# Kernel optimization log

Measured on AMD Instinct MI355X. Metric: run time of the kernel, lower is better.

Reference implementation:

```python
import jax, jax.numpy as jnp
import numpy as np

D = 128  # d_pair
N = 512  # n_res
B = 1
EPS = 1e-5


def setup_inputs() -> dict:
    key = jax.random.key(0)
    ks = jax.random.split(key, 16)
    s = 0.02
    inp = {
        "pair": jax.random.normal(ks[0], (B, N, N, D), dtype=jnp.float32),
        "pair_mask": jnp.ones((B, N, N), dtype=jnp.float32),
        "ln_g": jnp.ones((D,), dtype=jnp.float32),
        "ln_b": jnp.zeros((D,), dtype=jnp.float32),
        "w_lp": jax.random.normal(ks[1], (D, D), dtype=jnp.float32) * s,
        "b_lp": jnp.zeros((D,), dtype=jnp.float32),
        "w_lg": jax.random.normal(ks[2], (D, D), dtype=jnp.float32) * s,
        "b_lg": jnp.zeros((D,), dtype=jnp.float32),
        "w_rp": jax.random.normal(ks[3], (D, D), dtype=jnp.float32) * s,
        "b_rp": jnp.zeros((D,), dtype=jnp.float32),
        "w_rg": jax.random.normal(ks[4], (D, D), dtype=jnp.float32) * s,
        "b_rg": jnp.zeros((D,), dtype=jnp.float32),
        "w_g": jax.random.normal(ks[5], (D, D), dtype=jnp.float32) * s,
        "b_g": jnp.zeros((D,), dtype=jnp.float32),
        "w_o": jax.random.normal(ks[6], (D, D), dtype=jnp.float32) * s,
        "b_o": jnp.zeros((D,), dtype=jnp.float32),
    }
    return inp


def _layer_norm(x, g, b):
    mu = jnp.mean(x, axis=-1, keepdims=True)
    var = jnp.mean(jnp.square(x - mu), axis=-1, keepdims=True)
    return (x - mu) * jax.lax.rsqrt(var + EPS) * g + b


def reference(pair, pair_mask, ln_g, ln_b, w_lp, b_lp, w_lg, b_lg,
              w_rp, b_rp, w_rg, b_rg, w_g, b_g, w_o, b_o):
    # [B,N,N,D] pair representation; outgoing triangle multiplication
    x = _layer_norm(pair, ln_g, ln_b)
    mask = pair_mask[..., None]  # [B,N,N,1]
    left = (x @ w_lp + b_lp) * jax.nn.sigmoid(x @ w_lg + b_lg) * mask
    right = (x @ w_rp + b_rp) * jax.nn.sigmoid(x @ w_rg + b_rg) * mask
    # outgoing: contract over j -> per-channel NxN matmul
    out = jnp.einsum('bijd,bjkd->bikd', left, right)
    out = out * jax.nn.sigmoid(x @ w_g + b_g)
    out = out @ w_o + b_o
    return out
```

## Files before the change

### kernel.cpp

```cpp
#include <hip/hip_runtime.h>

#define NN 512
#define DD 128
#define PP (NN*NN)

typedef __attribute__((ext_vector_type(8))) short short8;
typedef __attribute__((ext_vector_type(4))) short shortx4;
typedef __attribute__((ext_vector_type(4))) float floatx4;
typedef __attribute__((ext_vector_type(4))) unsigned int uintx4;

__device__ __forceinline__ unsigned short f2bf(float f) {
  unsigned int u = __float_as_uint(f);
  u += 0x7fffu + ((u >> 16) & 1u);
  return (unsigned short)(u >> 16);
}
__device__ __forceinline__ float bf2f(unsigned short h) {
  return __uint_as_float(((unsigned int)h) << 16);
}
__device__ __forceinline__ unsigned int pkbf2(float lo, float hi) {
  unsigned int r;
  asm("v_cvt_pk_bf16_f32 %0, %1, %2" : "=v"(r) : "v"(lo), "v"(hi));
  return r;
}
__device__ __forceinline__ float sigm(float x) {
  return 1.f / (1.f + __expf(-x));
}

__device__ __forceinline__ void gload_lds16(const unsigned short* g, unsigned short* l) {
  __builtin_amdgcn_global_load_lds(
      (const __attribute__((address_space(1))) unsigned int*)g,
      (__attribute__((address_space(3))) unsigned int*)l, 16, 0, 0);
}

__global__ void k0_prep(const float* __restrict__ wlp, const float* __restrict__ wlg,
                        const float* __restrict__ wrp, const float* __restrict__ wrg,
                        const float* __restrict__ wg,  const float* __restrict__ wo,
                        unsigned short* __restrict__ wt) {
  const float* src[6] = {wlp, wlg, wrp, wrg, wg, wo};
  int m = blockIdx.y;
  int idx = blockIdx.x * 256 + threadIdx.x;
  int d = idx >> 7, e = idx & 127;
  wt[m * 16384 + e * 128 + d] = f2bf(src[m][d * 128 + e]);
}

__launch_bounds__(256, 4)
__global__ void k1a_ln(const float* __restrict__ pair,
                       const float* __restrict__ lng, const float* __restrict__ lnb,
                       unsigned short* __restrict__ xln) {
  const int t = threadIdx.x;
  const long p0 = (long)blockIdx.x << 7;
  const int r = t >> 1, h = t & 1;
  const float* row = pair + (p0 + r) * DD + h * 64;
  floatx4 v[16];
  float s = 0.f, s2 = 0.f;
  #pragma unroll
  for (int c = 0; c < 16; ++c) {
    v[c] = *(const floatx4*)(row + c * 4);
    s  += v[c].x + v[c].y + v[c].z + v[c].w;
    s2 += v[c].x * v[c].x + v[c].y * v[c].y + v[c].z * v[c].z + v[c].w * v[c].w;
  }
  s  += __shfl_xor(s, 1);
  s2 += __shfl_xor(s2, 1);
  float mu = s * (1.f / 128.f);
  float var = s2 * (1.f / 128.f) - mu * mu;
  float rs = rsqrtf(var + 1e-5f);
  unsigned short* orow = xln + (p0 + r) * DD + h * 64;
  #pragma unroll
  for (int c2 = 0; c2 < 8; ++c2) {
    floatx4 g0 = *(const floatx4*)(lng + h * 64 + c2 * 8);
    floatx4 g1 = *(const floatx4*)(lng + h * 64 + c2 * 8 + 4);
    floatx4 b0 = *(const floatx4*)(lnb + h * 64 + c2 * 8);
    floatx4 b1 = *(const floatx4*)(lnb + h * 64 + c2 * 8 + 4);
    floatx4 a = v[2 * c2], b = v[2 * c2 + 1];
    uintx4 u;
    u[0] = pkbf2((a.x - mu) * rs * g0.x + b0.x, (a.y - mu) * rs * g0.y + b0.y);
    u[1] = pkbf2((a.z - mu) * rs * g0.z + b0.z, (a.w - mu) * rs * g0.w + b0.w);
    u[2] = pkbf2((b.x - mu) * rs * g1.x + b1.x, (b.y - mu) * rs * g1.y + b1.y);
    u[3] = pkbf2((b.z - mu) * rs * g1.z + b1.z, (b.w - mu) * rs * g1.w + b1.w);
    *(uintx4*)(orow + c2 * 8) = u;
  }
}

__launch_bounds__(256, 2)
__global__ void k1b_proj(const unsigned short* __restrict__ xln,
                         const float* __restrict__ pmask,
                         const unsigned short* __restrict__ wt,
                         const float* __restrict__ b_lp, const float* __restrict__ b_lg,
                         const float* __restrict__ b_rp, const float* __restrict__ b_rg,
                         const float* __restrict__ b_g,
                         unsigned short* __restrict__ left_t,
                         unsigned short* __restrict__ right_bt,
                         unsigned short* __restrict__ gate_t) {
  __shared__ __align__(16) unsigned short Sm[17408];
  __shared__ float Mlds[128];
  unsigned short* Al = Sm;
  unsigned short* Bp = Sm + 4096;
  unsigned short* Bg = Sm + 8192;

  const int t = threadIdx.x;
  const int unit = blockIdx.y;
  const int q = blockIdx.x;

  int j0 = 0, kk = 0;
  long p0 = 0, soff;
  if (unit == 1) {
    j0 = (q >> 9) << 7; kk = q & 511;
    soff = (long)kk * NN + j0;
  } else {
    p0 = (long)q << 7;
    soff = p0;
  }
  auto arow = [&](int r) -> long {
    return (unit == 1) ? ((long)(j0 + r) * NN + kk) : (p0 + r);
  };

  if (unit < 2 && t < 128) Mlds[t] = pmask[arow(t)];

  const unsigned short* wA = wt + (unit == 0 ? 0 : unit == 1 ? 2 : 4) * 16384;
  const unsigned short* wB = wt + (unit == 0 ? 1 : 3) * 16384;

  const int lane = t & 63, w = t >> 6;
  const int ln = lane & 15, q8 = lane >> 4;
  const int wm = (w >> 1) << 6, we = (w & 1) << 6;
  const int sr = t >> 2, sc = t & 3;

  floatx4 aP[4][4] = {}, aG[4][4] = {};
  for (int kc = 0; kc < 4; ++kc) {
    gload_lds16(xln + arow(sr) * DD + kc * 32 + sc * 8,      &Al[t * 8]);
    gload_lds16(xln + arow(sr + 64) * DD + kc * 32 + sc * 8, &Al[(256 + t) * 8]);
    gload_lds16(wA + sr * 128 + kc * 32 + sc * 8,            &Bp[t * 8]);
    gload_lds16(wA + (sr + 64) * 128 + kc * 32 + sc * 8,     &Bp[(256 + t) * 8]);
    if (unit < 2) {
      gload_lds16(wB + sr * 128 + kc * 32 + sc * 8,          &Bg[t * 8]);
      gload_lds16(wB + (sr + 64) * 128 + kc * 32 + sc * 8,   &Bg[(256 + t) * 8]);
    }
    __syncthreads();
    short8 a[4];
    #pragma unroll
    for (int i = 0; i < 4; ++i)
      a[i] = *(const short8*)&Al[(wm + i * 16 + ln) * 32 + q8 * 8];
    #pragma unroll
    for (int j = 0; j < 4; ++j) {
      short8 bpv = *(const short8*)&Bp[(we + j * 16 + ln) * 32 + q8 * 8];
      #pragma unroll
      for (int i = 0; i < 4; ++i)
        aP[i][j] = __builtin_amdgcn_mfma_f32_16x16x32_bf16(a[i], bpv, aP[i][j], 0, 0, 0);
    }
    if (unit < 2) {
      #pragma unroll
      for (int j = 0; j < 4; ++j) {
        short8 bgv = *(const short8*)&Bg[(we + j * 16 + ln) * 32 + q8 * 8];
        #pragma unroll
        for (int i = 0; i < 4; ++i)
          aG[i][j] = __builtin_amdgcn_mfma_f32_16x16x32_bf16(a[i], bgv, aG[i][j], 0, 0, 0);
      }
    }
    __syncthreads();
  }

  unsigned short* mystg = Sm + w * 4352;
  if (unit < 2) {
    const float* bpp = (unit == 0) ? b_lp : b_rp;
    const float* bgg = (unit == 0) ? b_lg : b_rg;
    #pragma unroll
    for (int j = 0; j < 4; ++j) {
      int eg = we + j * 16 + ln;
      float bp = bpp[eg], bg = bgg[eg];
      #pragma unroll
      for (int i = 0; i < 4; ++i) {
        float vv[4];
        #pragma unroll
        for (int r = 0; r < 4; ++r) {
          int m = wm + i * 16 + q8 * 4 + r;
          vv[r] = (aP[i][j][r] + bp) * sigm(aG[i][j][r] + bg) * Mlds[m];
        }
        unsigned int* du = (unsigned int*)&mystg[(j * 16 + ln) * 68 + i * 16 + q8 * 4];
        du[0] = pkbf2(vv[0], vv[1]);
        du[1] = pkbf2(vv[2], vv[3]);
      }
    }
  } else {
    #pragma unroll
    for (int j = 0; j < 4; ++j) {
      int eg = we + j * 16 + ln;
      float bg = b_g[eg];
      #pragma unroll
      for (int i = 0; i < 4; ++i) {
        float vv[4];
        #pragma unroll
        for (int r = 0; r < 4; ++r)
          vv[r] = sigm(aP[i][j][r] + bg);
        unsigned int* du = (unsigned int*)&mystg[(j * 16 + ln) * 68 + i * 16 + q8 * 4];
        du[0] = pkbf2(vv[0], vv[1]);
        du[1] = pkbf2(vv[2], vv[3]);
      }
    }
  }

  unsigned short* dstbase = (unit == 0) ? left_t : (unit == 1 ? right_bt : gate_t);
  #pragma unroll
  for (int itr = 0; itr < 8; ++itr) {
    int row = itr * 8 + (lane >> 3);
    int c = lane & 7;
    short8 vv = *(const short8*)&mystg[row * 68 + c * 8];
    long eg = we + row;
    *(short8*)(dstbase + eg * PP + soff + wm + c * 8) = vv;
  }
}

__launch_bounds__(256, 3)
__global__ void k2_einsum(const unsigned short* __restrict__ left_t,
                          const unsigned short* __restrict__ right_bt,
                          unsigned short* __restrict__ tmpg) {
  __shared__ __align__(16) unsigned short Sm[128 * 132];
  unsigned short* Al = Sm;
  unsigned short* Bl = Sm + 128 * 32;
  unsigned short* Cl = Sm;
  const int t = threadIdx.x;
  const int d = blockIdx.y;
  const int i0 = (blockIdx.x >> 2) << 7;
  const int k0 = (blockIdx.x & 3) << 7;
  const unsigned short* Ag = left_t   + (long)d * PP;
  const unsigned short* Bg = right_bt + (long)d * PP;
  const int lane = t & 63, w = t >> 6;
  const int ln = lane & 15, q8 = lane >> 4;
  const int wm = (w >> 1) << 6, wn = (w & 1) << 6;

  floatx4 acc[4][4] = {};
  for (int j0 = 0; j0 < NN; j0 += 32) {
    #pragma unroll
    for (int it = 0; it < 2; ++it) {
      int flat = it * 256 + t;
      int r = flat >> 2, c = flat & 3;
      gload_lds16(Ag + (long)(i0 + r) * NN + j0 + c * 8, &Al[flat * 8]);
    }
    #pragma unroll
    for (int it = 0; it < 2; ++it) {
      int flat = it * 256 + t;
      int r = flat >> 2, c = flat & 3;
      gload_lds16(Bg + (long)(k0 + r) * NN + j0 + c * 8, &Bl[flat * 8]);
    }
    __syncthreads();
    short8 a[4], b[4];
    #pragma unroll
    for (int i = 0; i < 4; ++i)
      a[i] = *(const short8*)&Al[(wm + i * 16 + ln) * 32 + q8 * 8];
    #pragma unroll
    for (int i = 0; i < 4; ++i)
      b[i] = *(const short8*)&Bl[(wn + i * 16 + ln) * 32 + q8 * 8];
    #pragma unroll
    for (int i = 0; i < 4; ++i)
      #pragma unroll
      for (int j = 0; j < 4; ++j)
        acc[i][j] = __builtin_amdgcn_mfma_f32_16x16x32_bf16(a[i], b[j], acc[i][j], 0, 0, 0);
    __syncthreads();
  }
  #pragma unroll
  for (int i = 0; i < 4; ++i)
    #pragma unroll
    for (int j = 0; j < 4; ++j) {
      int n = wn + j * 16 + ln;
      #pragma unroll
      for (int r = 0; r < 4; ++r)
        Cl[(wm + i * 16 + q8 * 4 + r) * 132 + n] = f2bf(acc[i][j][r]);
    }
  __syncthreads();
  unsigned short* Og = tmpg + (long)d * PP;
  #pragma unroll
  for (int it = 0; it < 8; ++it) {
    int flat = it * 256 + t;
    int m = flat >> 4, c = flat & 15;
    *(short8*)(Og + (long)(i0 + m) * NN + k0 + c * 8) = *(const short8*)&Cl[m * 132 + c * 8];
  }
}

__launch_bounds__(256, 3)
__global__ void k3_out(const unsigned short* __restrict__ tmpg,
                       const unsigned short* __restrict__ gate_t,
                       const unsigned short* __restrict__ wt,
                       const float* __restrict__ b_o,
                       float* __restrict__ out) {
  __shared__ __align__(16) unsigned short Tl[128 * 144];
  unsigned int* TlU = (unsigned int*)Tl;
  const int t = threadIdx.x;
  const long p0 = (long)blockIdx.x << 7;
  const unsigned short* wo = wt + 5 * 16384;

  #pragma unroll
  for (int it = 0; it < 4; ++it) {
    int flat = it * 256 + t;
    int rp = flat >> 4;
    int c  = flat & 15;
    const unsigned short* ra = tmpg   + (long)(2 * rp) * PP + p0 + c * 8;
    const unsigned short* ga = gate_t + (long)(2 * rp) * PP + p0 + c * 8;
    uintx4 xa = *(const uintx4*)ra;
    uintx4 xb = *(const uintx4*)(ra + PP);
    uintx4 ya = *(const uintx4*)ga;
    uintx4 yb = *(const uintx4*)(ga + PP);
    #pragma unroll
    for (int cc = 0; cc < 4; ++cc) {
      float pl = __uint_as_float(xa[cc] << 16) * __uint_as_float(ya[cc] << 16);
      float ph = __uint_as_float(xa[cc] & 0xffff0000u) * __uint_as_float(ya[cc] & 0xffff0000u);
      float ql = __uint_as_float(xb[cc] << 16) * __uint_as_float(yb[cc] << 16);
      float qh = __uint_as_float(xb[cc] & 0xffff0000u) * __uint_as_float(yb[cc] & 0xffff0000u);
      int p = c * 8 + 2 * cc;
      TlU[p * 72 + rp]       = pkbf2(pl, ql);
      TlU[(p + 1) * 72 + rp] = pkbf2(ph, qh);
    }
  }
  __syncthreads();

  const int lane = t & 63, w = t >> 6;
  const int ln = lane & 15, q8 = lane >> 4;
  const int wm = (w >> 1) << 6, wn = (w & 1) << 6;

  floatx4 acc[4][4] = {};
  #pragma unroll
  for (int ks = 0; ks < 4; ++ks) {
    short8 a[4], b[4];
    #pragma unroll
    for (int i = 0; i < 4; ++i)
      a[i] = *(const short8*)&Tl[(wm + i * 16 + ln) * 144 + ks * 32 + q8 * 8];
    #pragma unroll
    for (int j = 0; j < 4; ++j)
      b[j] = *(const short8*)(wo + (wn + j * 16 + ln) * 128 + ks * 32 + q8 * 8);
    #pragma unroll
    for (int i = 0; i < 4; ++i)
      #pragma unroll
      for (int j = 0; j < 4; ++j)
        acc[i][j] = __builtin_amdgcn_mfma_f32_16x16x32_bf16(a[i], b[j], acc[i][j], 0, 0, 0);
  }
  #pragma unroll
  for (int j = 0; j < 4; ++j) {
    int eg = wn + j * 16 + ln;
    float bias = b_o[eg];
    #pragma unroll
    for (int i = 0; i < 4; ++i)
      #pragma unroll
      for (int r = 0; r < 4; ++r) {
        int m = wm + i * 16 + q8 * 4 + r;
        out[(p0 + m) * DD + eg] = acc[i][j][r] + bias;
      }
  }
}

extern "C" void kernel_launch(void* const* d_in, const int* in_sizes, int n_in,
                              void* d_out, int out_size, void* d_ws, size_t ws_size,
                              hipStream_t stream) {
  const float* pair = (const float*)d_in[0];
  const float* pmask = (const float*)d_in[1];
  const float* ln_g = (const float*)d_in[2];
  const float* ln_b = (const float*)d_in[3];
  const float* w_lp = (const float*)d_in[4];
  const float* b_lp = (const float*)d_in[5];
  const float* w_lg = (const float*)d_in[6];
  const float* b_lg = (const float*)d_in[7];
  const float* w_rp = (const float*)d_in[8];
  const float* b_rp = (const float*)d_in[9];
  const float* w_rg = (const float*)d_in[10];
  const float* b_rg = (const float*)d_in[11];
  const float* w_g  = (const float*)d_in[12];
  const float* b_g  = (const float*)d_in[13];
  const float* w_o  = (const float*)d_in[14];
  const float* b_o  = (const float*)d_in[15];
  float* out = (float*)d_out;

  char* ws = (char*)d_ws;
  unsigned short* wt       = (unsigned short*)ws;
  unsigned short* xln      = (unsigned short*)(ws + 196608);
  unsigned short* left_t   = xln      + (size_t)PP * DD;
  unsigned short* right_bt = left_t   + (size_t)PP * DD;
  unsigned short* gate_t   = right_bt + (size_t)PP * DD;
  unsigned short* tmpg     = xln;

  k0_prep<<<dim3(64, 6), 256, 0, stream>>>(w_lp, w_lg, w_rp, w_rg, w_g, w_o, wt);
  k1a_ln<<<dim3(2048), 256, 0, stream>>>(pair, ln_g, ln_b, xln);
  k1b_proj<<<dim3(2048, 3), 256, 0, stream>>>(xln, pmask, wt,
      b_lp, b_lg, b_rp, b_rg, b_g, left_t, right_bt, gate_t);
  k2_einsum<<<dim3(16, 128), 256, 0, stream>>>(left_t, right_bt, tmpg);
  k3_out<<<dim3(2048), 256, 0, stream>>>(tmpg, gate_t, wt, b_o, out);
}
```

Baseline: 518.4 us.

## Use 512-thread blocks with 8 waves and swizzle k3 LDS transpose

Doubles the block size of the projection, einsum and output kernels to 512 threads. Each of the eight waves now computes a 64x32 sub-tile instead of 64x64, which halves accumulator registers per wave and lets more waves hide latency. The k3_out kernel also gets an XOR swizzle on its transposed LDS writes and reads to cut bank conflicts. The cost is less MFMA work per LDS load per wave and more barrier participants per block.

```diff
diff --git a/kernel.cpp b/kernel.cpp
--- a/kernel.cpp
+++ b/kernel.cpp
@@ -5,7 +5,6 @@
 #define PP (NN*NN)
 
 typedef __attribute__((ext_vector_type(8))) short short8;
-typedef __attribute__((ext_vector_type(4))) short shortx4;
 typedef __attribute__((ext_vector_type(4))) float floatx4;
 typedef __attribute__((ext_vector_type(4))) unsigned int uintx4;
 
@@ -13,9 +12,6 @@
   unsigned int u = __float_as_uint(f);
   u += 0x7fffu + ((u >> 16) & 1u);
   return (unsigned short)(u >> 16);
-}
-__device__ __forceinline__ float bf2f(unsigned short h) {
-  return __uint_as_float(((unsigned int)h) << 16);
 }
 __device__ __forceinline__ unsigned int pkbf2(float lo, float hi) {
   unsigned int r;
@@ -81,7 +77,7 @@
   }
 }
 
-__launch_bounds__(256, 2)
+__launch_bounds__(512, 4)
 __global__ void k1b_proj(const unsigned short* __restrict__ xln,
                          const float* __restrict__ pmask,
                          const unsigned short* __restrict__ wt,
@@ -121,26 +117,22 @@
 
   const int lane = t & 63, w = t >> 6;
   const int ln = lane & 15, q8 = lane >> 4;
-  const int wm = (w >> 1) << 6, we = (w & 1) << 6;
+  const int wm = (w >> 2) << 6, we = (w & 3) << 5;
   const int sr = t >> 2, sc = t & 3;
 
-  floatx4 aP[4][4] = {}, aG[4][4] = {};
+  floatx4 aP[4][2] = {}, aG[4][2] = {};
   for (int kc = 0; kc < 4; ++kc) {
-    gload_lds16(xln + arow(sr) * DD + kc * 32 + sc * 8,      &Al[t * 8]);
-    gload_lds16(xln + arow(sr + 64) * DD + kc * 32 + sc * 8, &Al[(256 + t) * 8]);
-    gload_lds16(wA + sr * 128 + kc * 32 + sc * 8,            &Bp[t * 8]);
-    gload_lds16(wA + (sr + 64) * 128 + kc * 32 + sc * 8,     &Bp[(256 + t) * 8]);
-    if (unit < 2) {
-      gload_lds16(wB + sr * 128 + kc * 32 + sc * 8,          &Bg[t * 8]);
-      gload_lds16(wB + (sr + 64) * 128 + kc * 32 + sc * 8,   &Bg[(256 + t) * 8]);
-    }
+    gload_lds16(xln + arow(sr) * DD + kc * 32 + sc * 8, &Al[t * 8]);
+    gload_lds16(wA + sr * 128 + kc * 32 + sc * 8,       &Bp[t * 8]);
+    if (unit < 2)
+      gload_lds16(wB + sr * 128 + kc * 32 + sc * 8,     &Bg[t * 8]);
     __syncthreads();
     short8 a[4];
     #pragma unroll
     for (int i = 0; i < 4; ++i)
       a[i] = *(const short8*)&Al[(wm + i * 16 + ln) * 32 + q8 * 8];
     #pragma unroll
-    for (int j = 0; j < 4; ++j) {
+    for (int j = 0; j < 2; ++j) {
       short8 bpv = *(const short8*)&Bp[(we + j * 16 + ln) * 32 + q8 * 8];
       #pragma unroll
       for (int i = 0; i < 4; ++i)
@@ -148,7 +140,7 @@
     }
     if (unit < 2) {
       #pragma unroll
-      for (int j = 0; j < 4; ++j) {
+      for (int j = 0; j < 2; ++j) {
         short8 bgv = *(const short8*)&Bg[(we + j * 16 + ln) * 32 + q8 * 8];
         #pragma unroll
         for (int i = 0; i < 4; ++i)
@@ -158,12 +150,12 @@
     __syncthreads();
   }
 
-  unsigned short* mystg = Sm + w * 4352;
+  unsigned short* mystg = Sm + w * 2176;
   if (unit < 2) {
     const float* bpp = (unit == 0) ? b_lp : b_rp;
     const float* bgg = (unit == 0) ? b_lg : b_rg;
     #pragma unroll
-    for (int j = 0; j < 4; ++j) {
+    for (int j = 0; j < 2; ++j) {
       int eg = we + j * 16 + ln;
       float bp = bpp[eg], bg = bgg[eg];
       #pragma unroll
@@ -181,7 +173,7 @@
     }
   } else {
     #pragma unroll
-    for (int j = 0; j < 4; ++j) {
+    for (int j = 0; j < 2; ++j) {
       int eg = we + j * 16 + ln;
       float bg = b_g[eg];
       #pragma unroll
@@ -199,7 +191,7 @@
 
   unsigned short* dstbase = (unit == 0) ? left_t : (unit == 1 ? right_bt : gate_t);
   #pragma unroll
-  for (int itr = 0; itr < 8; ++itr) {
+  for (int itr = 0; itr < 4; ++itr) {
     int row = itr * 8 + (lane >> 3);
     int c = lane & 7;
     short8 vv = *(const short8*)&mystg[row * 68 + c * 8];
@@ -208,7 +200,7 @@
   }
 }
 
-__launch_bounds__(256, 3)
+__launch_bounds__(512, 4)
 __global__ void k2_einsum(const unsigned short* __restrict__ left_t,
                           const unsigned short* __restrict__ right_bt,
                           unsigned short* __restrict__ tmpg) {
@@ -224,41 +216,32 @@
   const unsigned short* Bg = right_bt + (long)d * PP;
   const int lane = t & 63, w = t >> 6;
   const int ln = lane & 15, q8 = lane >> 4;
-  const int wm = (w >> 1) << 6, wn = (w & 1) << 6;
-
-  floatx4 acc[4][4] = {};
+  const int wm = (w >> 2) << 6, wn = (w & 3) << 5;
+  const int sr = t >> 2, sc = t & 3;
+
+  floatx4 acc[4][2] = {};
   for (int j0 = 0; j0 < NN; j0 += 32) {
-    #pragma unroll
-    for (int it = 0; it < 2; ++it) {
-      int flat = it * 256 + t;
-      int r = flat >> 2, c = flat & 3;
-      gload_lds16(Ag + (long)(i0 + r) * NN + j0 + c * 8, &Al[flat * 8]);
-    }
-    #pragma unroll
-    for (int it = 0; it < 2; ++it) {
-      int flat = it * 256 + t;
-      int r = flat >> 2, c = flat & 3;
-      gload_lds16(Bg + (long)(k0 + r) * NN + j0 + c * 8, &Bl[flat * 8]);
-    }
+    gload_lds16(Ag + (long)(i0 + sr) * NN + j0 + sc * 8, &Al[t * 8]);
+    gload_lds16(Bg + (long)(k0 + sr) * NN + j0 + sc * 8, &Bl[t * 8]);
     __syncthreads();
-    short8 a[4], b[4];
+    short8 a[4], b[2];
     #pragma unroll
     for (int i = 0; i < 4; ++i)
       a[i] = *(const short8*)&Al[(wm + i * 16 + ln) * 32 + q8 * 8];
     #pragma unroll
-    for (int i = 0; i < 4; ++i)
-      b[i] = *(const short8*)&Bl[(wn + i * 16 + ln) * 32 + q8 * 8];
-    #pragma unroll
-    for (int i = 0; i < 4; ++i)
-      #pragma unroll
-      for (int j = 0; j < 4; ++j)
+    for (int j = 0; j < 2; ++j)
+      b[j] = *(const short8*)&Bl[(wn + j * 16 + ln) * 32 + q8 * 8];
+    #pragma unroll
+    for (int i = 0; i < 4; ++i)
+      #pragma unroll
+      for (int j = 0; j < 2; ++j)
         acc[i][j] = __builtin_amdgcn_mfma_f32_16x16x32_bf16(a[i], b[j], acc[i][j], 0, 0, 0);
     __syncthreads();
   }
   #pragma unroll
   for (int i = 0; i < 4; ++i)
     #pragma unroll
-    for (int j = 0; j < 4; ++j) {
+    for (int j = 0; j < 2; ++j) {
       int n = wn + j * 16 + ln;
       #pragma unroll
       for (int r = 0; r < 4; ++r)
@@ -267,14 +250,14 @@
   __syncthreads();
   unsigned short* Og = tmpg + (long)d * PP;
   #pragma unroll
-  for (int it = 0; it < 8; ++it) {
-    int flat = it * 256 + t;
+  for (int it = 0; it < 4; ++it) {
+    int flat = it * 512 + t;
     int m = flat >> 4, c = flat & 15;
     *(short8*)(Og + (long)(i0 + m) * NN + k0 + c * 8) = *(const short8*)&Cl[m * 132 + c * 8];
   }
 }
 
-__launch_bounds__(256, 3)
+__launch_bounds__(512, 4)
 __global__ void k3_out(const unsigned short* __restrict__ tmpg,
                        const unsigned short* __restrict__ gate_t,
                        const unsigned short* __restrict__ wt,
@@ -287,8 +270,8 @@
   const unsigned short* wo = wt + 5 * 16384;
 
   #pragma unroll
-  for (int it = 0; it < 4; ++it) {
-    int flat = it * 256 + t;
+  for (int it = 0; it < 2; ++it) {
+    int flat = it * 512 + t;
     int rp = flat >> 4;
     int c  = flat & 15;
     const unsigned short* ra = tmpg   + (long)(2 * rp) * PP + p0 + c * 8;
@@ -297,6 +280,7 @@
     uintx4 xb = *(const uintx4*)(ra + PP);
     uintx4 ya = *(const uintx4*)ga;
     uintx4 yb = *(const uintx4*)(ga + PP);
+    int sw = ((c & 7) << 3) ^ ((c >> 3) << 2);
     #pragma unroll
     for (int cc = 0; cc < 4; ++cc) {
       float pl = __uint_as_float(xa[cc] << 16) * __uint_as_float(ya[cc] << 16);
@@ -304,34 +288,37 @@
       float ql = __uint_as_float(xb[cc] << 16) * __uint_as_float(yb[cc] << 16);
       float qh = __uint_as_float(xb[cc] & 0xffff0000u) * __uint_as_float(yb[cc] & 0xffff0000u);
       int p = c * 8 + 2 * cc;
-      TlU[p * 72 + rp]       = pkbf2(pl, ql);
-      TlU[(p + 1) * 72 + rp] = pkbf2(ph, qh);
+      TlU[p * 72 + (rp ^ sw)]       = pkbf2(pl, ql);
+      TlU[(p + 1) * 72 + (rp ^ sw)] = pkbf2(ph, qh);
     }
   }
   __syncthreads();
 
   const int lane = t & 63, w = t >> 6;
   const int ln = lane & 15, q8 = lane >> 4;
-  const int wm = (w >> 1) << 6, wn = (w & 1) << 6;
-
-  floatx4 acc[4][4] = {};
+  const int wm = (w >> 2) << 6, wn = (w & 3) << 5;
+
+  floatx4 acc[4][2] = {};
   #pragma unroll
   for (int ks = 0; ks < 4; ++ks) {
-    short8 a[4], b[4];
-    #pragma unroll
-    for (int i = 0; i < 4; ++i)
-      a[i] = *(const short8*)&Tl[(wm + i * 16 + ln) * 144 + ks * 32 + q8 * 8];
-    #pragma unroll
-    for (int j = 0; j < 4; ++j)
+    short8 a[4], b[2];
+    #pragma unroll
+    for (int i = 0; i < 4; ++i) {
+      int p = wm + i * 16 + ln;
+      int swh = (((p >> 3) & 7) << 4) ^ (((p >> 6) & 1) << 3);
+      a[i] = *(const short8*)&Tl[p * 144 + ((ks * 32 + q8 * 8) ^ swh)];
+    }
+    #pragma unroll
+    for (int j = 0; j < 2; ++j)
       b[j] = *(const short8*)(wo + (wn + j * 16 + ln) * 128 + ks * 32 + q8 * 8);
     #pragma unroll
     for (int i = 0; i < 4; ++i)
       #pragma unroll
-      for (int j = 0; j < 4; ++j)
+      for (int j = 0; j < 2; ++j)
         acc[i][j] = __builtin_amdgcn_mfma_f32_16x16x32_bf16(a[i], b[j], acc[i][j], 0, 0, 0);
   }
   #pragma unroll
-  for (int j = 0; j < 4; ++j) {
+  for (int j = 0; j < 2; ++j) {
     int eg = wn + j * 16 + ln;
     float bias = b_o[eg];
     #pragma unroll
@@ -375,8 +362,8 @@
 
   k0_prep<<<dim3(64, 6), 256, 0, stream>>>(w_lp, w_lg, w_rp, w_rg, w_g, w_o, wt);
   k1a_ln<<<dim3(2048), 256, 0, stream>>>(pair, ln_g, ln_b, xln);
-  k1b_proj<<<dim3(2048, 3), 256, 0, stream>>>(xln, pmask, wt,
+  k1b_proj<<<dim3(2048, 3), 512, 0, stream>>>(xln, pmask, wt,
       b_lp, b_lg, b_rp, b_rg, b_g, left_t, right_bt, gate_t);
-  k2_einsum<<<dim3(16, 128), 256, 0, stream>>>(left_t, right_bt, tmpg);
-  k3_out<<<dim3(2048), 256, 0, stream>>>(tmpg, gate_t, wt, b_o, out);
-}
+  k2_einsum<<<dim3(16, 128), 512, 0, stream>>>(left_t, right_bt, tmpg);
+  k3_out<<<dim3(2048), 512, 0, stream>>>(tmpg, gate_t, wt, b_o, out);
+}
```

After: 518.2 us. About the same (-0.0%).
